# Optimization experiments

Measured on AMD Instinct MI355X. Metric: run time of the kernel, lower is better.

Reference implementation:

```python
import jax, jax.numpy as jnp
import numpy as np

T, B, Q, H = 100, 256, 2048, 1024  # steps, students, n_questions, n_hidden
NIN = 2 * Q                         # n_input = 2 * n_questions


def setup_inputs() -> dict:
    key = jax.random.key(0)
    ks = jax.random.split(key, 8)
    s = 0.02  # init scale
    return {
        "x_idx": jax.random.randint(ks[0], (T, B), 0, NIN),          # one-hot index into 2Q
        "y_idx": jax.random.randint(ks[1], (T, B), 0, Q),             # next-question one-hot index
        "truth": (jax.random.uniform(ks[2], (T, B)) > 0.5).astype(jnp.float32),
        "Wm": jax.random.normal(ks[3], (H, H), jnp.float32) * s,
        "bm": jnp.zeros((H,), jnp.float32),
        "Wx": jax.random.normal(ks[4], (H, NIN), jnp.float32) * s,
        "bx": jnp.zeros((H,), jnp.float32),
        "Wy": jax.random.normal(ks[5], (Q, H), jnp.float32) * s,
        "by": jnp.zeros((Q,), jnp.float32),
        "W_start": jax.random.normal(ks[6], (H, 1), jnp.float32) * s,
        "b_start": jnp.zeros((H,), jnp.float32),
    }


def reference(x_idx, y_idx, truth, Wm, bm, Wx, bx, Wy, by, W_start, b_start):
    # state = start(zeros(B,1)): zeros @ W_start^T + b_start -> [B, H]
    h0 = jnp.zeros((B, 1), Wm.dtype) @ W_start.T + b_start

    # lin_x(input_x) with one-hot input_x == column-select of Wx: [T, B, H]
    xproj = Wx.T[x_idx] + bx

    def step(h, xp):
        h = jnp.tanh(h @ Wm.T + bm + xp)  # Elman cell: tanh(lin_m(h) + lin_x(x))
        return h, h

    _, hiddens = jax.lax.scan(step, h0, xproj)  # hiddens: [T, B, H]

    # pred = sum(sigmoid(lin_y(h)) * y_onehot) == sigmoid(logit at y_idx)
    Wy_sel = Wy[y_idx]                                        # [T, B, H]
    logits = jnp.einsum('tbh,tbh->tb', hiddens, Wy_sel) + by[y_idx]
    pred = jax.nn.sigmoid(logits)                             # [T, B]

    # BCELoss(reduction='none'): -(t*log(p) + (1-t)*log(1-p)); stable via log_sigmoid
    loss = -(truth * jax.nn.log_sigmoid(logits) + (1.0 - truth) * jax.nn.log_sigmoid(-logits))
    return pred, loss
```

## Files before the change

### kernel.cpp

```cpp
#include <hip/hip_runtime.h>
#include <hip/hip_bf16.h>
#include <math.h>

#define T_STEPS 100
#define B 256
#define Q 2048
#define H 1024
#define NIN 4096

typedef __attribute__((ext_vector_type(8))) short bf16x8;
typedef __attribute__((ext_vector_type(4))) short bf16x4;
typedef __attribute__((ext_vector_type(4))) float f32x4;
typedef unsigned long long u64;

#define HLDS0_OFF 0
#define HLDS1_OFF 16384
#define HOUT_OFF  32768
#define LOGIT_OFF (32768 + 2048)
#define SMEM_BYTES (LOGIT_OFF + 256)

#define H0_OFF 0
#define H1_OFF (512 * 1024)
#define LP_OFF (1024 * 1024)
#define FLAG_OFF (LP_OFF + 1638400)

#define AGENT __HIP_MEMORY_SCOPE_AGENT

__device__ inline unsigned short f2bf(float f) {
    union { float f; unsigned int u; } c; c.f = f;
    unsigned int u = c.u + 0x7fffu + ((c.u >> 16) & 1u);
    return (unsigned short)(u >> 16);
}

__global__ void ws_init(unsigned* __restrict__ flags) {
    int idx = blockIdx.x * blockDim.x + threadIdx.x;
    if (idx < 16 * 64) flags[idx] = 0u;
}

__global__ __launch_bounds__(256, 1) void rnn_persistent(
    const int* __restrict__ x_idx, const int* __restrict__ y_idx,
    const float* __restrict__ truth,
    const float* __restrict__ Wm, const float* __restrict__ bm,
    const float* __restrict__ Wx, const float* __restrict__ bx_,
    const float* __restrict__ Wy, const float* __restrict__ by,
    const float* __restrict__ b_start,
    __hip_bfloat16* __restrict__ h0buf, __hip_bfloat16* __restrict__ h1buf,
    float* __restrict__ lp, unsigned* __restrict__ flags,
    float* __restrict__ out)
{
    extern __shared__ char lds[];

    const int tid = threadIdx.x;
    const int bid = blockIdx.x;
    const int rg = bid & 15;
    const int sg = bid >> 4;
    const int sbase = sg * 16;
    const int w  = tid >> 6;
    const int l  = tid & 63;
    const int lr = l & 15;
    const int g  = l >> 4;

    unsigned* sgf = flags + sg * 64;

    bf16x8 a_frag[32];
    {
        const int row = rg * 64 + w * 16 + lr;
        const float* wrow = &Wm[(size_t)row * H];
        #pragma unroll
        for (int half = 0; half < 2; ++half) {
            #pragma unroll
            for (int kk = 0; kk < 16; ++kk) {
                int k0 = (half * 64 + kk * 4 + g) * 8;
                float4 v0 = *reinterpret_cast<const float4*>(&wrow[k0]);
                float4 v1 = *reinterpret_cast<const float4*>(&wrow[k0 + 4]);
                bf16x8 f;
                f[0] = (short)f2bf(v0.x); f[1] = (short)f2bf(v0.y);
                f[2] = (short)f2bf(v0.z); f[3] = (short)f2bf(v0.w);
                f[4] = (short)f2bf(v1.x); f[5] = (short)f2bf(v1.y);
                f[6] = (short)f2bf(v1.z); f[7] = (short)f2bf(v1.w);
                a_frag[half * 16 + kk] = f;
            }
        }
    }
    {
        int s = tid >> 4, c8 = tid & 15;
        union { unsigned short s4[4]; u64 u; } pk;
        #pragma unroll
        for (int e = 0; e < 4; ++e) pk.s4[e] = f2bf(b_start[rg * 64 + c8 * 4 + e]);
        __hip_atomic_store((u64*)&h0buf[(size_t)(sbase + s) * H + rg * 64 + c8 * 4],
                           pk.u, __ATOMIC_RELAXED, AGENT);
    }
    float bias_r[4];
    #pragma unroll
    for (int r = 0; r < 4; ++r) {
        int gi = rg * 64 + w * 16 + g * 4 + r;
        bias_r[r] = bm[gi] + bx_[gi];
    }
    float wx_r[4], wy_r[4];
    {
        int xc = x_idx[sbase + lr];
        int yc = y_idx[sbase + lr];
        #pragma unroll
        for (int r = 0; r < 4; ++r) {
            int gi = rg * 64 + w * 16 + g * 4 + r;
            wx_r[r] = Wx[(size_t)gi * NIN + xc];
            wy_r[r] = Wy[(size_t)yc * H + gi];
        }
    }

    {
        asm volatile("s_waitcnt vmcnt(0)" ::: "memory");
        __syncthreads();
        if (tid == 0) __hip_atomic_store(&sgf[rg], 1u, __ATOMIC_RELAXED, AGENT);
        if (rg == 0) {
            if (tid < 64) {
                unsigned v;
                do {
                    v = (tid < 16) ? __hip_atomic_load(&sgf[tid], __ATOMIC_RELAXED, AGENT) : 1u;
                } while (!__all(v >= 1u));
                if (tid == 0) __hip_atomic_store(&sgf[32], 1u, __ATOMIC_RELAXED, AGENT);
            }
        } else if (tid == 0) {
            while (__hip_atomic_load(&sgf[32], __ATOMIC_RELAXED, AGENT) < 1u) {}
        }
        __syncthreads();
    }

    for (int t = 0; t < T_STEPS; ++t) {
        const __hip_bfloat16* hc = (t & 1) ? h1buf : h0buf;
        __hip_bfloat16*       hn = (t & 1) ? h0buf : h1buf;

        u64 r0[8], r1[8];
        #pragma unroll
        for (int it = 0; it < 4; ++it) {
            int q = it * 256 + tid;
            int srow = q >> 6, sl = q & 63;
            const u64* src = (const u64*)&hc[(size_t)(sbase + srow) * H + sl * 8];
            r0[2 * it]     = __hip_atomic_load(src,     __ATOMIC_RELAXED, AGENT);
            r0[2 * it + 1] = __hip_atomic_load(src + 1, __ATOMIC_RELAXED, AGENT);
        }
        #pragma unroll
        for (int it = 0; it < 4; ++it) {
            int q = it * 256 + tid;
            int srow = q >> 6, sl = q & 63;
            const u64* src = (const u64*)&hc[(size_t)(sbase + srow) * H + 512 + sl * 8];
            r1[2 * it]     = __hip_atomic_load(src,     __ATOMIC_RELAXED, AGENT);
            r1[2 * it + 1] = __hip_atomic_load(src + 1, __ATOMIC_RELAXED, AGENT);
        }

        #pragma unroll
        for (int it = 0; it < 4; ++it) {
            int q = it * 256 + tid;
            int srow = q >> 6, sl = q & 63;
            union { u64 u[2]; bf16x8 v; } cvt;
            cvt.u[0] = r0[2 * it]; cvt.u[1] = r0[2 * it + 1];
            *reinterpret_cast<bf16x8*>(
                &lds[HLDS0_OFF + srow * 1024 + ((sl ^ (srow & 7)) << 4)]) = cvt.v;
        }
        #pragma unroll
        for (int it = 0; it < 4; ++it) {
            int q = it * 256 + tid;
            int srow = q >> 6, sl = q & 63;
            union { u64 u[2]; bf16x8 v; } cvt;
            cvt.u[0] = r1[2 * it]; cvt.u[1] = r1[2 * it + 1];
            *reinterpret_cast<bf16x8*>(
                &lds[HLDS1_OFF + srow * 1024 + ((sl ^ (srow & 7)) << 4)]) = cvt.v;
        }
        __syncthreads();

        f32x4 acc = {0.f, 0.f, 0.f, 0.f};
        #pragma unroll
        for (int kk = 0; kk < 16; ++kk) {
            bf16x8 bb = *reinterpret_cast<const bf16x8*>(
                &lds[HLDS0_OFF + lr * 1024 + (((kk * 4 + g) ^ (lr & 7)) << 4)]);
            acc = __builtin_amdgcn_mfma_f32_16x16x32_bf16(a_frag[kk], bb, acc, 0, 0, 0);
        }
        #pragma unroll
        for (int kk = 0; kk < 16; ++kk) {
            bf16x8 bb = *reinterpret_cast<const bf16x8*>(
                &lds[HLDS1_OFF + lr * 1024 + (((kk * 4 + g) ^ (lr & 7)) << 4)]);
            acc = __builtin_amdgcn_mfma_f32_16x16x32_bf16(a_frag[16 + kk], bb, acc, 0, 0, 0);
        }

        float hv[4];
        #pragma unroll
        for (int r = 0; r < 4; ++r)
            hv[r] = tanhf(acc[r] + bias_r[r] + wx_r[r]);

        {
            int row0  = w * 16 + g * 4;
            int chunk = row0 >> 3;
            bf16x4 b4;
            b4[0] = (short)f2bf(hv[0]); b4[1] = (short)f2bf(hv[1]);
            b4[2] = (short)f2bf(hv[2]); b4[3] = (short)f2bf(hv[3]);
            int byte = HOUT_OFF + lr * 128 + ((chunk ^ (lr & 7)) << 4) + ((row0 & 7) << 1);
            *reinterpret_cast<bf16x4*>(&lds[byte]) = b4;
        }
        {
            float p = hv[0] * wy_r[0] + hv[1] * wy_r[1] + hv[2] * wy_r[2] + hv[3] * wy_r[3];
            p += __shfl_down(p, 32);
            p += __shfl_down(p, 16);
            if (l < 16)
                *reinterpret_cast<float*>(&lds[LOGIT_OFF + (w * 16 + l) * 4]) = p;
        }
        __syncthreads();
        {
            int s = tid >> 4, c8 = tid & 15;
            u64 v = *reinterpret_cast<const u64*>(
                &lds[HOUT_OFF + s * 128 + (((c8 >> 1) ^ (s & 7)) << 4) + ((c8 & 1) << 3)]);
            __hip_atomic_store((u64*)&hn[(size_t)(sbase + s) * H + rg * 64 + c8 * 4],
                               v, __ATOMIC_RELAXED, AGENT);
        }
        if (tid < 16) {
            const float* lg = reinterpret_cast<const float*>(&lds[LOGIT_OFF]);
            float ps = lg[tid] + lg[16 + tid] + lg[32 + tid] + lg[48 + tid];
            __hip_atomic_store(&lp[(size_t)(t * 16 + rg) * B + sbase + tid],
                               ps, __ATOMIC_RELAXED, AGENT);
        }

        {
            const unsigned fval = (unsigned)(t + 2);
            asm volatile("s_waitcnt vmcnt(0)" ::: "memory");
            __syncthreads();
            if (tid == 0) __hip_atomic_store(&sgf[rg], fval, __ATOMIC_RELAXED, AGENT);

            {
                int tn = (t + 1 < T_STEPS) ? t + 1 : t;
                int xc = x_idx[tn * B + sbase + lr];
                int yc = y_idx[tn * B + sbase + lr];
                #pragma unroll
                for (int r = 0; r < 4; ++r) {
                    int gi = rg * 64 + w * 16 + g * 4 + r;
                    wx_r[r] = Wx[(size_t)gi * NIN + xc];
                    wy_r[r] = Wy[(size_t)yc * H + gi];
                }
            }

            if (rg == 0) {
                if (tid < 64) {
                    unsigned v;
                    do {
                        v = (tid < 16) ? __hip_atomic_load(&sgf[tid], __ATOMIC_RELAXED, AGENT) : fval;
                    } while (!__all(v >= fval));
                    if (tid == 0) __hip_atomic_store(&sgf[32], fval, __ATOMIC_RELAXED, AGENT);
                }
            } else if (tid == 0) {
                while (__hip_atomic_load(&sgf[32], __ATOMIC_RELAXED, AGENT) < fval) {}
            }
            __syncthreads();
        }
    }

    {
        int ti = tid >> 4, s = tid & 15;
        int t = rg + ti * 16;
        if (t < T_STEPS) {
            int idx = t * B + sbase + s;
            float lgv = 0.f;
            #pragma unroll
            for (int rgi = 0; rgi < 16; ++rgi)
                lgv += __hip_atomic_load(&lp[(size_t)(t * 16 + rgi) * B + sbase + s],
                                         __ATOMIC_RELAXED, AGENT);
            int yc = y_idx[idx];
            lgv += by[yc];
            float pred = 1.f / (1.f + expf(-lgv));
            float tv = truth[idx];
            float e = log1pf(expf(-fabsf(lgv)));
            float ls_pos = fminf(lgv, 0.f) - e;
            float ls_neg = fminf(-lgv, 0.f) - e;
            out[idx] = pred;
            out[T_STEPS * B + idx] = -(tv * ls_pos + (1.f - tv) * ls_neg);
        }
    }
}

extern "C" void kernel_launch(void* const* d_in, const int* in_sizes, int n_in,
                              void* d_out, int out_size, void* d_ws, size_t ws_size,
                              hipStream_t stream) {
    const int*   x_idx   = (const int*)d_in[0];
    const int*   y_idx   = (const int*)d_in[1];
    const float* truth   = (const float*)d_in[2];
    const float* Wm      = (const float*)d_in[3];
    const float* bm      = (const float*)d_in[4];
    const float* Wx      = (const float*)d_in[5];
    const float* bx_     = (const float*)d_in[6];
    const float* Wy      = (const float*)d_in[7];
    const float* by      = (const float*)d_in[8];
    const float* b_start = (const float*)d_in[10];
    float* out = (float*)d_out;

    __hip_bfloat16* h0buf = (__hip_bfloat16*)((char*)d_ws + H0_OFF);
    __hip_bfloat16* h1buf = (__hip_bfloat16*)((char*)d_ws + H1_OFF);
    float*          lp    = (float*)((char*)d_ws + LP_OFF);
    unsigned*       flags = (unsigned*)((char*)d_ws + FLAG_OFF);

    ws_init<<<4, 256, 0, stream>>>(flags);

    rnn_persistent<<<dim3(256), dim3(256), SMEM_BYTES, stream>>>(
        x_idx, y_idx, truth, Wm, bm, Wx, bx_, Wy, by, b_start,
        h0buf, h1buf, lp, flags, out);
}
```

Measured before the change: 420.8 us.

## Replace leader-relay barrier with per-block flag polling and direct h stores

Each block's first wave now polls all 16 sibling flags itself and releases the rest of the block through an LDS go flag. This replaces the old scheme, where group leader rg==0 polled and then republished a shared flag, and it removes one __syncthreads per step. The hidden-state output is written straight from registers to global memory instead of being staged through LDS. The MFMA chain is split across two accumulators to shorten dependency latency. The trade-offs are more polling traffic on the global flags and less coalesced 8-byte stores, and the LDS spin on a volatile flag with no barrier depends on the ordering being correct.

```diff
diff --git a/kernel.cpp b/kernel.cpp
--- a/kernel.cpp
+++ b/kernel.cpp
@@ -9,15 +9,14 @@
 #define NIN 4096
 
 typedef __attribute__((ext_vector_type(8))) short bf16x8;
-typedef __attribute__((ext_vector_type(4))) short bf16x4;
 typedef __attribute__((ext_vector_type(4))) float f32x4;
 typedef unsigned long long u64;
 
 #define HLDS0_OFF 0
 #define HLDS1_OFF 16384
-#define HOUT_OFF  32768
-#define LOGIT_OFF (32768 + 2048)
-#define SMEM_BYTES (LOGIT_OFF + 256)
+#define LOGIT_OFF 32768
+#define GO_OFF    (32768 + 256)
+#define SMEM_BYTES (GO_OFF + 16)
 
 #define H0_OFF 0
 #define H1_OFF (512 * 1024)
@@ -34,7 +33,7 @@
 
 __global__ void ws_init(unsigned* __restrict__ flags) {
     int idx = blockIdx.x * blockDim.x + threadIdx.x;
-    if (idx < 16 * 64) flags[idx] = 0u;
+    if (idx < 16 * 16) flags[idx] = 0u;
 }
 
 __global__ __launch_bounds__(256, 1) void rnn_persistent(
@@ -60,7 +59,10 @@
     const int lr = l & 15;
     const int g  = l >> 4;
 
-    unsigned* sgf = flags + sg * 64;
+    unsigned* sgf = flags + sg * 16;
+    volatile unsigned* go_lds = (volatile unsigned*)&lds[GO_OFF];
+
+    if (tid == 0) *go_lds = 0u;
 
     bf16x8 a_frag[32];
     {
@@ -112,18 +114,14 @@
         asm volatile("s_waitcnt vmcnt(0)" ::: "memory");
         __syncthreads();
         if (tid == 0) __hip_atomic_store(&sgf[rg], 1u, __ATOMIC_RELAXED, AGENT);
-        if (rg == 0) {
-            if (tid < 64) {
-                unsigned v;
-                do {
-                    v = (tid < 16) ? __hip_atomic_load(&sgf[tid], __ATOMIC_RELAXED, AGENT) : 1u;
-                } while (!__all(v >= 1u));
-                if (tid == 0) __hip_atomic_store(&sgf[32], 1u, __ATOMIC_RELAXED, AGENT);
-            }
-        } else if (tid == 0) {
-            while (__hip_atomic_load(&sgf[32], __ATOMIC_RELAXED, AGENT) < 1u) {}
-        }
-        __syncthreads();
+        if (w == 0) {
+            unsigned v;
+            do { v = (l < 16) ? __hip_atomic_load(&sgf[l], __ATOMIC_RELAXED, AGENT) : 1u; }
+            while (!__all(v >= 1u));
+            if (tid == 0) *go_lds = 1u;
+        } else {
+            while (*go_lds < 1u) {}
+        }
     }
 
     for (int t = 0; t < T_STEPS; ++t) {
@@ -168,33 +166,39 @@
         }
         __syncthreads();
 
-        f32x4 acc = {0.f, 0.f, 0.f, 0.f};
-        #pragma unroll
-        for (int kk = 0; kk < 16; ++kk) {
-            bf16x8 bb = *reinterpret_cast<const bf16x8*>(
-                &lds[HLDS0_OFF + lr * 1024 + (((kk * 4 + g) ^ (lr & 7)) << 4)]);
-            acc = __builtin_amdgcn_mfma_f32_16x16x32_bf16(a_frag[kk], bb, acc, 0, 0, 0);
-        }
-        #pragma unroll
-        for (int kk = 0; kk < 16; ++kk) {
-            bf16x8 bb = *reinterpret_cast<const bf16x8*>(
-                &lds[HLDS1_OFF + lr * 1024 + (((kk * 4 + g) ^ (lr & 7)) << 4)]);
-            acc = __builtin_amdgcn_mfma_f32_16x16x32_bf16(a_frag[16 + kk], bb, acc, 0, 0, 0);
+        f32x4 acc0 = {0.f, 0.f, 0.f, 0.f};
+        f32x4 acc1 = {0.f, 0.f, 0.f, 0.f};
+        #pragma unroll
+        for (int kk = 0; kk < 16; kk += 2) {
+            bf16x8 b0 = *reinterpret_cast<const bf16x8*>(
+                &lds[HLDS0_OFF + lr * 1024 + ((((kk    ) * 4 + g) ^ (lr & 7)) << 4)]);
+            acc0 = __builtin_amdgcn_mfma_f32_16x16x32_bf16(a_frag[kk],     b0, acc0, 0, 0, 0);
+            bf16x8 b1 = *reinterpret_cast<const bf16x8*>(
+                &lds[HLDS0_OFF + lr * 1024 + ((((kk + 1) * 4 + g) ^ (lr & 7)) << 4)]);
+            acc1 = __builtin_amdgcn_mfma_f32_16x16x32_bf16(a_frag[kk + 1], b1, acc1, 0, 0, 0);
+        }
+        #pragma unroll
+        for (int kk = 0; kk < 16; kk += 2) {
+            bf16x8 b0 = *reinterpret_cast<const bf16x8*>(
+                &lds[HLDS1_OFF + lr * 1024 + ((((kk    ) * 4 + g) ^ (lr & 7)) << 4)]);
+            acc0 = __builtin_amdgcn_mfma_f32_16x16x32_bf16(a_frag[16 + kk],     b0, acc0, 0, 0, 0);
+            bf16x8 b1 = *reinterpret_cast<const bf16x8*>(
+                &lds[HLDS1_OFF + lr * 1024 + ((((kk + 1) * 4 + g) ^ (lr & 7)) << 4)]);
+            acc1 = __builtin_amdgcn_mfma_f32_16x16x32_bf16(a_frag[16 + kk + 1], b1, acc1, 0, 0, 0);
         }
 
         float hv[4];
         #pragma unroll
         for (int r = 0; r < 4; ++r)
-            hv[r] = tanhf(acc[r] + bias_r[r] + wx_r[r]);
+            hv[r] = tanhf(acc0[r] + acc1[r] + bias_r[r] + wx_r[r]);
 
         {
-            int row0  = w * 16 + g * 4;
-            int chunk = row0 >> 3;
-            bf16x4 b4;
-            b4[0] = (short)f2bf(hv[0]); b4[1] = (short)f2bf(hv[1]);
-            b4[2] = (short)f2bf(hv[2]); b4[3] = (short)f2bf(hv[3]);
-            int byte = HOUT_OFF + lr * 128 + ((chunk ^ (lr & 7)) << 4) + ((row0 & 7) << 1);
-            *reinterpret_cast<bf16x4*>(&lds[byte]) = b4;
+            union { unsigned short s4[4]; u64 u; } pk;
+            #pragma unroll
+            for (int r = 0; r < 4; ++r) pk.s4[r] = f2bf(hv[r]);
+            __hip_atomic_store(
+                (u64*)&hn[(size_t)(sbase + lr) * H + rg * 64 + w * 16 + g * 4],
+                pk.u, __ATOMIC_RELAXED, AGENT);
         }
         {
             float p = hv[0] * wy_r[0] + hv[1] * wy_r[1] + hv[2] * wy_r[2] + hv[3] * wy_r[3];
@@ -204,13 +208,6 @@
                 *reinterpret_cast<float*>(&lds[LOGIT_OFF + (w * 16 + l) * 4]) = p;
         }
         __syncthreads();
-        {
-            int s = tid >> 4, c8 = tid & 15;
-            u64 v = *reinterpret_cast<const u64*>(
-                &lds[HOUT_OFF + s * 128 + (((c8 >> 1) ^ (s & 7)) << 4) + ((c8 & 1) << 3)]);
-            __hip_atomic_store((u64*)&hn[(size_t)(sbase + s) * H + rg * 64 + c8 * 4],
-                               v, __ATOMIC_RELAXED, AGENT);
-        }
         if (tid < 16) {
             const float* lg = reinterpret_cast<const float*>(&lds[LOGIT_OFF]);
             float ps = lg[tid] + lg[16 + tid] + lg[32 + tid] + lg[48 + tid];
@@ -236,18 +233,14 @@
                 }
             }
 
-            if (rg == 0) {
-                if (tid < 64) {
-                    unsigned v;
-                    do {
-                        v = (tid < 16) ? __hip_atomic_load(&sgf[tid], __ATOMIC_RELAXED, AGENT) : fval;
-                    } while (!__all(v >= fval));
-                    if (tid == 0) __hip_atomic_store(&sgf[32], fval, __ATOMIC_RELAXED, AGENT);
-                }
-            } else if (tid == 0) {
-                while (__hip_atomic_load(&sgf[32], __ATOMIC_RELAXED, AGENT) < fval) {}
+            if (w == 0) {
+                unsigned v;
+                do { v = (l < 16) ? __hip_atomic_load(&sgf[l], __ATOMIC_RELAXED, AGENT) : fval; }
+                while (!__all(v >= fval));
+                if (tid == 0) *go_lds = fval;
+            } else {
+                while (*go_lds < fval) {}
             }
-            __syncthreads();
         }
     }
 
@@ -294,7 +287,7 @@
     float*          lp    = (float*)((char*)d_ws + LP_OFF);
     unsigned*       flags = (unsigned*)((char*)d_ws + FLAG_OFF);
 
-    ws_init<<<4, 256, 0, stream>>>(flags);
+    ws_init<<<1, 256, 0, stream>>>(flags);
 
     rnn_persistent<<<dim3(256), dim3(256), SMEM_BYTES, stream>>>(
         x_idx, y_idx, truth, Wm, bm, Wx, bx_, Wy, by, b_start,
```

After: 450.4 us. +7.0%, slower.
